# Kernel tuning notes

Hardware: AMD Instinct MI355X
Metric: run time of the kernel (lower is better)

## Reference

```python
import jax, jax.numpy as jnp
import numpy as np

N, C, T, V, H, O = 64, 256, 64, 25, 3, 256
D = max(C // 8, 8)  # rel_channels = 32
BN_EPS = 1e-5


def setup_inputs() -> dict:
    key = jax.random.key(0)
    ks = jax.random.split(key, 12)
    x = jax.random.normal(ks[0], (N, C, T, V), jnp.float32)
    # binary skeleton-style prior adjacency per head + derived 2-hop
    rng = np.random.RandomState(0)
    A = (rng.rand(H, V, V) < 0.15).astype(np.float32)
    A2 = np.zeros_like(A)
    for h in range(H):
        A2[h] = np.clip(np.minimum(A[h] @ A[h], 1.0) - A[h], 0.0, 1.0)
    s = 1.0 / np.sqrt(C)
    return {
        "x": x,
        "A_prior": jnp.asarray(A),
        "A_2hop": jnp.asarray(A2),
        "beta": jnp.float32(0.3),
        "lam": jnp.float32(0.5),
        "W_phi": jax.random.normal(ks[1], (H * D, C), jnp.float32) * s,
        "b_phi": jnp.zeros((H * D,), jnp.float32),
        "W_psi": jax.random.normal(ks[2], (H * D, C), jnp.float32) * s,
        "b_psi": jnp.zeros((H * D,), jnp.float32),
        "W_d": jax.random.normal(ks[3], (H, O, C), jnp.float32) * s,
        "b_d": jnp.zeros((H, O), jnp.float32),
        "bn_gamma": jnp.ones((O,), jnp.float32),
        "bn_beta": jnp.zeros((O,), jnp.float32),
        "bn_mean": jax.random.normal(ks[4], (O,), jnp.float32) * 0.1,
        "bn_var": jax.random.uniform(ks[5], (O,), jnp.float32, 0.5, 1.5),
        "W_g": jax.random.normal(ks[6], (O, C), jnp.float32) * s,
        "b_g": jnp.zeros((O,), jnp.float32),
    }


def reference(x, A_prior, A_2hop, beta, lam, W_phi, b_phi, W_psi, b_psi,
              W_d, b_d, bn_gamma, bn_beta, bn_mean, bn_var, W_g, b_g):
    n, c, t, v = x.shape
    h = A_prior.shape[0]
    d = W_phi.shape[0] // h
    scale = d ** -0.5

    def conv1x1_heads(W, b):
        # n c t v -> (n t) h v d
        y = jnp.einsum('nctv,ec->netv', x, W) + b[None, :, None, None]
        return y.reshape(n, h, d, t, v).transpose(0, 3, 1, 4, 2).reshape(n * t, h, v, d)

    phi = conv1x1_heads(W_phi, b_phi)
    psi = conv1x1_heads(W_psi, b_psi)
    A_adapt = jax.nn.softmax(jnp.einsum('bhvd,bhwd->bhvw', phi, psi) * scale, axis=-1)

    lam_c = jnp.clip(lam, 0.0, 1.0)
    A_final = (A_prior + beta * A_2hop)[None] + lam_c * A_adapt  # [(n t), h, v, v]

    feat = x.transpose(0, 2, 3, 1).reshape(n * t, v, c)  # (n t) v c
    z = jnp.einsum('bhvw,bwc->bhvc', A_final, feat)       # per-head aggregation
    out = jnp.einsum('bhvc,hoc->bvo', z, W_d) + jnp.sum(b_d, axis=0)  # sum of per-head 1x1 convs
    out = out.reshape(n, t, v, -1).transpose(0, 3, 1, 2)  # n o t v

    # BatchNorm2d (inference form with running stats)
    inv = jax.lax.rsqrt(bn_var + BN_EPS)
    out = (out - bn_mean[None, :, None, None]) * (inv * bn_gamma)[None, :, None, None] + bn_beta[None, :, None, None]

    gate = jax.nn.sigmoid(jnp.einsum('nctv,oc->notv', x, W_g) + b_g[None, :, None, None])
    out = gate * out + x  # down is identity since in_channels == out_channels
    return jax.nn.relu(out)
```

## Files before the change

### kernel.cpp

```cpp
#include <hip/hip_runtime.h>
#include <math.h>

#define N_ 64
#define C_ 256
#define T_ 64
#define V_ 25
#define H_ 3
#define O_ 256
#define D_ 32
#define HD_ 96

using short8 = __attribute__((ext_vector_type(8))) short;
using f32x4  = __attribute__((ext_vector_type(4))) float;

#define WS_WD   0
#define WS_WG   196608
#define WS_WPHI 262144
#define WS_WPSI 286720

__device__ __forceinline__ unsigned short f2bf(float f) {
    unsigned int u = __float_as_uint(f);
    unsigned int r = (u + 0x7fffu + ((u >> 16) & 1u)) >> 16;
    return (unsigned short)r;
}

__global__ __launch_bounds__(256)
void prep_weights(const float* __restrict__ Wd, const float* __restrict__ Wg,
                  const float* __restrict__ Wphi, const float* __restrict__ Wpsi,
                  unsigned short* __restrict__ ws) {
    int gid = blockIdx.x * 256 + threadIdx.x;
    if (gid >= 608 * 64) return;
    int tile = gid >> 6, lane = gid & 63;
    int lcol = lane & 15, lrow = lane >> 4;
    const float* W;
    unsigned short* base;
    int ot, ks;
    if (tile < 384) {
        int h = tile >> 7, r = tile & 127;
        ot = r >> 3; ks = r & 7;
        W = Wd + (size_t)h * O_ * C_;
        base = ws + WS_WD + (size_t)tile * 512;
    } else if (tile < 512) {
        int r = tile - 384;
        ot = r >> 3; ks = r & 7;
        W = Wg;
        base = ws + WS_WG + (size_t)r * 512;
    } else if (tile < 560) {
        int r = tile - 512;
        ot = r >> 3; ks = r & 7;
        W = Wphi;
        base = ws + WS_WPHI + (size_t)r * 512;
    } else {
        int r = tile - 560;
        ot = r >> 3; ks = r & 7;
        W = Wpsi;
        base = ws + WS_WPSI + (size_t)r * 512;
    }
    int row = ot * 16 + lcol;
    int c0  = ks * 32 + lrow * 8;
    const float* s = W + (size_t)row * C_ + c0;
    unsigned int p[4];
    #pragma unroll
    for (int q = 0; q < 4; ++q) {
        unsigned short lo = f2bf(s[2 * q]);
        unsigned short hi = f2bf(s[2 * q + 1]);
        p[q] = (unsigned int)lo | ((unsigned int)hi << 16);
    }
    uint4 pk = make_uint4(p[0], p[1], p[2], p[3]);
    *(uint4*)(base + (size_t)lane * 8) = pk;
}

#define L_PHIT 16384
#define L_PSIT 26384
#define L_AFIN 36384
#define L_M    42528
#define L_TOT  63008

__global__ __launch_bounds__(256)
void hdgc_mfma(const float* __restrict__ x,
               const float* __restrict__ A_prior,
               const float* __restrict__ A_2hop,
               const float* __restrict__ beta_p,
               const float* __restrict__ lam_p,
               const float* __restrict__ b_phi,
               const float* __restrict__ b_psi,
               const unsigned short* __restrict__ ws,
               const float* __restrict__ b_d,
               const float* __restrict__ bn_gamma,
               const float* __restrict__ bn_beta,
               const float* __restrict__ bn_mean,
               const float* __restrict__ bn_var,
               const float* __restrict__ b_g,
               float* __restrict__ out) {
    __shared__ __align__(16) char lds[L_TOT];
    char*  xbT  = lds;
    float* phiT = (float*)(lds + L_PHIT);
    float* psiT = (float*)(lds + L_PSIT);
    char*  Afin = lds + L_AFIN;
    char*  Mlds = lds + L_M;
    float* Slds = (float*)(lds + L_M);

    const int tid  = threadIdx.x;
    const int lane = tid & 63, wid = tid >> 6;
    const int lcol = lane & 15, lrow = lane >> 4;
    const int b = blockIdx.x, n = b / T_, t = b - n * T_;
    const size_t xbase = (size_t)n * (C_ * T_ * V_) + (size_t)t * V_;

    for (int i = tid; i < 7 * 256; i += 256) {
        int v = 25 + (i >> 8), c = i & 255;
        *(unsigned short*)(xbT + (((v << 9) + (c << 1)) ^ ((v & 7) << 4))) = 0;
    }
    for (int i = tid; i < 3 * 32 * 32; i += 256)
        ((unsigned short*)Afin)[i] = 0;
    for (int i = tid; i < C_ * V_; i += 256) {
        int c = i / V_, v = i - c * V_;
        unsigned short bv = f2bf(x[xbase + (size_t)c * (T_ * V_) + v]);
        *(unsigned short*)(xbT + (((v << 9) + (c << 1)) ^ ((v & 7) << 4))) = bv;
    }
    __syncthreads();

    {
        const unsigned short* wsrc = ws + ((wid >> 1) ? WS_WPSI : WS_WPHI);
        const float* bias = (wid >> 1) ? b_psi : b_phi;
        float* dstT = (wid >> 1) ? psiT : phiT;
        int otbase = (wid & 1) * 3;
        f32x4 acc[3][2];
        #pragma unroll
        for (int oi = 0; oi < 3; ++oi)
            #pragma unroll
            for (int wt = 0; wt < 2; ++wt) acc[oi][wt] = (f32x4){0.f, 0.f, 0.f, 0.f};
        for (int ks = 0; ks < 8; ++ks) {
            const int cb = (ks * 32 + lrow * 8) << 1;
            short8 b0 = *(const short8*)(xbT + (((lcol << 9) + cb) ^ ((lcol & 7) << 4)));
            const int v1 = 16 + lcol;
            short8 b1 = *(const short8*)(xbT + (((v1 << 9) + cb) ^ ((v1 & 7) << 4)));
            #pragma unroll
            for (int oi = 0; oi < 3; ++oi) {
                int ot = otbase + oi;
                short8 a = *(const short8*)(wsrc + (((ot << 3) + ks) << 9) + lane * 8);
                acc[oi][0] = __builtin_amdgcn_mfma_f32_16x16x32_bf16(a, b0, acc[oi][0], 0, 0, 0);
                acc[oi][1] = __builtin_amdgcn_mfma_f32_16x16x32_bf16(a, b1, acc[oi][1], 0, 0, 0);
            }
        }
        #pragma unroll
        for (int oi = 0; oi < 3; ++oi) {
            int ot = otbase + oi;
            #pragma unroll
            for (int r = 0; r < 4; ++r) {
                int e = ot * 16 + lrow * 4 + r;
                float bv = bias[e];
                if (lcol < 25)      dstT[lcol * 100 + e]       = acc[oi][0][r] + bv;
                if (16 + lcol < 25) dstT[(16 + lcol) * 100 + e] = acc[oi][1][r] + bv;
            }
        }
    }
    __syncthreads();

    for (int it = tid; it < H_ * V_ * V_; it += 256) {
        int h = it / (V_ * V_), rem = it - h * V_ * V_;
        int v = rem / V_, w = rem - v * V_;
        const f32x4* pv = (const f32x4*)(phiT + v * 100 + h * 32);
        const f32x4* pw = (const f32x4*)(psiT + w * 100 + h * 32);
        float s = 0.f;
        #pragma unroll
        for (int q = 0; q < 8; ++q) {
            f32x4 a = pv[q], c = pw[q];
            s += a[0] * c[0] + a[1] * c[1] + a[2] * c[2] + a[3] * c[3];
        }
        Slds[(h * 25 + v) * 28 + w] = s * 0.17677669529663687f;
    }
    __syncthreads();

    if (tid < H_ * V_) {
        int h = tid / 25, v = tid - h * 25;
        float lam  = fminf(fmaxf(lam_p[0], 0.f), 1.f);
        float beta = beta_p[0];
        const float* row = Slds + tid * 28;
        float mx = -1e30f;
        #pragma unroll
        for (int w = 0; w < 25; ++w) mx = fmaxf(mx, row[w]);
        float e[25], sum = 0.f;
        #pragma unroll
        for (int w = 0; w < 25; ++w) { e[w] = __expf(row[w] - mx); sum += e[w]; }
        float sc = lam / sum;
        const float* Ap = A_prior + tid * 25;
        const float* A2 = A_2hop + tid * 25;
        #pragma unroll
        for (int w = 0; w < 25; ++w) {
            float af = Ap[w] + beta * A2[w] + sc * e[w];
            *(unsigned short*)(Afin + (((((h * 32 + v) << 6) + (w << 1))) ^ ((v & 7) << 4))) = f2bf(af);
        }
    }
    __syncthreads();

    f32x4 oacc[4][2], gacc[4][2];
    #pragma unroll
    for (int oi = 0; oi < 4; ++oi)
        #pragma unroll
        for (int vt = 0; vt < 2; ++vt) {
            oacc[oi][vt] = (f32x4){0.f, 0.f, 0.f, 0.f};
            gacc[oi][vt] = (f32x4){0.f, 0.f, 0.f, 0.f};
        }

    for (int h = 0; h < H_; ++h) {
        f32x4 macc[4][2];
        #pragma unroll
        for (int oi = 0; oi < 4; ++oi)
            #pragma unroll
            for (int wt = 0; wt < 2; ++wt) macc[oi][wt] = (f32x4){0.f, 0.f, 0.f, 0.f};
        for (int ks = 0; ks < 8; ++ks) {
            const int cb = (ks * 32 + lrow * 8) << 1;
            short8 b0 = *(const short8*)(xbT + (((lcol << 9) + cb) ^ ((lcol & 7) << 4)));
            const int v1 = 16 + lcol;
            short8 b1 = *(const short8*)(xbT + (((v1 << 9) + cb) ^ ((v1 & 7) << 4)));
            #pragma unroll
            for (int oi = 0; oi < 4; ++oi) {
                int ot = wid * 4 + oi;
                short8 a = *(const short8*)(ws + WS_WD + ((((h * 16 + ot) << 3) + ks) << 9) + lane * 8);
                macc[oi][0] = __builtin_amdgcn_mfma_f32_16x16x32_bf16(a, b0, macc[oi][0], 0, 0, 0);
                macc[oi][1] = __builtin_amdgcn_mfma_f32_16x16x32_bf16(a, b1, macc[oi][1], 0, 0, 0);
            }
        }
        #pragma unroll
        for (int oi = 0; oi < 4; ++oi) {
            int ot = wid * 4 + oi;
            #pragma unroll
            for (int r = 0; r < 4; ++r) {
                int o = ot * 16 + lrow * 4 + r;
                *(unsigned short*)(Mlds + o * 80 + (lcol << 1))        = f2bf(macc[oi][0][r]);
                *(unsigned short*)(Mlds + o * 80 + ((16 + lcol) << 1)) = f2bf(macc[oi][1][r]);
            }
        }
        __syncthreads();
        {
            short8 af[4];
            #pragma unroll
            for (int oi = 0; oi < 4; ++oi) {
                int ot = wid * 4 + oi;
                af[oi] = *(const short8*)(Mlds + (ot * 16 + lcol) * 80 + (lrow << 4));
            }
            #pragma unroll
            for (int vt = 0; vt < 2; ++vt) {
                int v = vt * 16 + lcol;
                short8 bf = *(const short8*)(Afin + ((((h * 32 + v) << 6) + (lrow << 4)) ^ ((v & 7) << 4)));
                #pragma unroll
                for (int oi = 0; oi < 4; ++oi)
                    oacc[oi][vt] = __builtin_amdgcn_mfma_f32_16x16x32_bf16(af[oi], bf, oacc[oi][vt], 0, 0, 0);
            }
        }
        __syncthreads();
    }

    for (int ks = 0; ks < 8; ++ks) {
        const int cb = (ks * 32 + lrow * 8) << 1;
        short8 b0 = *(const short8*)(xbT + (((lcol << 9) + cb) ^ ((lcol & 7) << 4)));
        const int v1 = 16 + lcol;
        short8 b1 = *(const short8*)(xbT + (((v1 << 9) + cb) ^ ((v1 & 7) << 4)));
        #pragma unroll
        for (int oi = 0; oi < 4; ++oi) {
            int ot = wid * 4 + oi;
            short8 a = *(const short8*)(ws + WS_WG + (((ot << 3) + ks) << 9) + lane * 8);
            gacc[oi][0] = __builtin_amdgcn_mfma_f32_16x16x32_bf16(a, b0, gacc[oi][0], 0, 0, 0);
            gacc[oi][1] = __builtin_amdgcn_mfma_f32_16x16x32_bf16(a, b1, gacc[oi][1], 0, 0, 0);
        }
    }

    #pragma unroll
    for (int oi = 0; oi < 4; ++oi) {
        int ot = wid * 4 + oi;
        #pragma unroll
        for (int r = 0; r < 4; ++r) {
            int o = ot * 16 + lrow * 4 + r;
            float bdsum = b_d[o] + b_d[O_ + o] + b_d[2 * O_ + o];
            float inv  = rsqrtf(bn_var[o] + 1e-5f) * bn_gamma[o];
            float mean = bn_mean[o], bnb = bn_beta[o], bg = b_g[o];
            float* op = out + xbase + (size_t)o * (T_ * V_);
            #pragma unroll
            for (int vt = 0; vt < 2; ++vt) {
                int v = vt * 16 + lcol;
                if (v < V_) {
                    float pre = (oacc[oi][vt][r] + bdsum - mean) * inv + bnb;
                    float gl  = gacc[oi][vt][r] + bg;
                    float g   = 1.f / (1.f + __expf(-gl));
                    unsigned short xb =
                        *(unsigned short*)(xbT + (((v << 9) + (o << 1)) ^ ((v & 7) << 4)));
                    float res = __uint_as_float(((unsigned int)xb) << 16);
                    float rr = g * pre + res;
                    op[v] = fmaxf(rr, 0.f);
                }
            }
        }
    }
}

extern "C" void kernel_launch(void* const* d_in, const int* in_sizes, int n_in,
                              void* d_out, int out_size, void* d_ws, size_t ws_size,
                              hipStream_t stream) {
    const float* x        = (const float*)d_in[0];
    const float* A_prior  = (const float*)d_in[1];
    const float* A_2hop   = (const float*)d_in[2];
    const float* beta_p   = (const float*)d_in[3];
    const float* lam_p    = (const float*)d_in[4];
    const float* W_phi    = (const float*)d_in[5];
    const float* b_phi    = (const float*)d_in[6];
    const float* W_psi    = (const float*)d_in[7];
    const float* b_psi    = (const float*)d_in[8];
    const float* W_d      = (const float*)d_in[9];
    const float* b_d      = (const float*)d_in[10];
    const float* bn_gamma = (const float*)d_in[11];
    const float* bn_beta  = (const float*)d_in[12];
    const float* bn_mean  = (const float*)d_in[13];
    const float* bn_var   = (const float*)d_in[14];
    const float* W_g      = (const float*)d_in[15];
    const float* b_g      = (const float*)d_in[16];
    unsigned short* ws = (unsigned short*)d_ws;
    float* out = (float*)d_out;

    hipLaunchKernelGGL(prep_weights, dim3(152), dim3(256), 0, stream,
                       W_d, W_g, W_phi, W_psi, ws);
    hipLaunchKernelGGL(hdgc_mfma, dim3(N_ * T_), dim3(256), 0, stream,
                       x, A_prior, A_2hop, beta_p, lam_p,
                       b_phi, b_psi, ws,
                       b_d, bn_gamma, bn_beta, bn_mean, bn_var, b_g, out);
}
```

Before: 464.6 us.

## Compute phi·psi scores with bf16 MFMA and shrink LDS footprint

Stores phi/psi projections as bf16 in a shared scratch region and computes the per-head 25x25 attention scores with four 16x16x32 bf16 MFMAs per head, replacing the scalar fp32 dot-product loop. The LDS layout is compacted by overlapping the phi/psi/score scratch with the later M buffer, which reduces per-block shared memory and may allow more resident blocks. The x staging loop now packs two channels per 32-bit store. Rounding phi/psi to bf16 adds precision loss in the softmax logits.

After: 515.0 us. 1.11x slower.

```diff
diff --git a/kernel.cpp b/kernel.cpp
--- a/kernel.cpp
+++ b/kernel.cpp
@@ -70,11 +70,13 @@
     *(uint4*)(base + (size_t)lane * 8) = pk;
 }
 
-#define L_PHIT 16384
-#define L_PSIT 26384
-#define L_AFIN 36384
-#define L_M    42528
-#define L_TOT  63008
+#define L_AFIN 16384
+#define L_SCR  22528
+#define L_PHIB L_SCR
+#define L_PSIB (L_SCR + 6656)
+#define L_S    (L_SCR + 13312)
+#define L_M    L_SCR
+#define L_TOT  44240
 
 __global__ __launch_bounds__(256)
 void hdgc_mfma(const float* __restrict__ x,
@@ -93,12 +95,12 @@
                const float* __restrict__ b_g,
                float* __restrict__ out) {
     __shared__ __align__(16) char lds[L_TOT];
-    char*  xbT  = lds;
-    float* phiT = (float*)(lds + L_PHIT);
-    float* psiT = (float*)(lds + L_PSIT);
-    char*  Afin = lds + L_AFIN;
-    char*  Mlds = lds + L_M;
-    float* Slds = (float*)(lds + L_M);
+    char*           xbT  = lds;
+    char*           Afin = lds + L_AFIN;
+    unsigned short* phiB = (unsigned short*)(lds + L_PHIB);
+    unsigned short* psiB = (unsigned short*)(lds + L_PSIB);
+    float*          Slds = (float*)(lds + L_S);
+    char*           Mlds = lds + L_M;
 
     const int tid  = threadIdx.x;
     const int lane = tid & 63, wid = tid >> 6;
@@ -112,17 +114,20 @@
     }
     for (int i = tid; i < 3 * 32 * 32; i += 256)
         ((unsigned short*)Afin)[i] = 0;
-    for (int i = tid; i < C_ * V_; i += 256) {
-        int c = i / V_, v = i - c * V_;
-        unsigned short bv = f2bf(x[xbase + (size_t)c * (T_ * V_) + v]);
-        *(unsigned short*)(xbT + (((v << 9) + (c << 1)) ^ ((v & 7) << 4))) = bv;
+    for (int i = tid; i < 128 * V_; i += 256) {
+        int p = i / V_, v = i - p * V_;
+        int c = p * 2;
+        const float* xs = x + xbase + (size_t)c * (T_ * V_) + v;
+        unsigned int lo = f2bf(xs[0]);
+        unsigned int hi = f2bf(xs[T_ * V_]);
+        *(unsigned int*)(xbT + (((v << 9) + (c << 1)) ^ ((v & 7) << 4))) = lo | (hi << 16);
     }
     __syncthreads();
 
     {
         const unsigned short* wsrc = ws + ((wid >> 1) ? WS_WPSI : WS_WPHI);
         const float* bias = (wid >> 1) ? b_psi : b_phi;
-        float* dstT = (wid >> 1) ? psiT : phiT;
+        unsigned short* dstB = (wid >> 1) ? psiB : phiB;
         int otbase = (wid & 1) * 3;
         f32x4 acc[3][2];
         #pragma unroll
@@ -149,25 +154,40 @@
             for (int r = 0; r < 4; ++r) {
                 int e = ot * 16 + lrow * 4 + r;
                 float bv = bias[e];
-                if (lcol < 25)      dstT[lcol * 100 + e]       = acc[oi][0][r] + bv;
-                if (16 + lcol < 25) dstT[(16 + lcol) * 100 + e] = acc[oi][1][r] + bv;
+                if (lcol < 25) dstB[lcol * 104 + e]        = f2bf(acc[oi][0][r] + bv);
+                if (lcol < 9)  dstB[(16 + lcol) * 104 + e] = f2bf(acc[oi][1][r] + bv);
             }
         }
     }
     __syncthreads();
 
-    for (int it = tid; it < H_ * V_ * V_; it += 256) {
-        int h = it / (V_ * V_), rem = it - h * V_ * V_;
-        int v = rem / V_, w = rem - v * V_;
-        const f32x4* pv = (const f32x4*)(phiT + v * 100 + h * 32);
-        const f32x4* pw = (const f32x4*)(psiT + w * 100 + h * 32);
-        float s = 0.f;
-        #pragma unroll
-        for (int q = 0; q < 8; ++q) {
-            f32x4 a = pv[q], c = pw[q];
-            s += a[0] * c[0] + a[1] * c[1] + a[2] * c[2] + a[3] * c[3];
-        }
-        Slds[(h * 25 + v) * 28 + w] = s * 0.17677669529663687f;
+    if (wid < H_) {
+        const int h = wid;
+        const int eo = h * 32 + lrow * 8;
+        short8 a0 = *(const short8*)(phiB + lcol * 104 + eo);
+        short8 a1 = *(const short8*)(phiB + (16 + lcol) * 104 + eo);
+        short8 q0 = *(const short8*)(psiB + lcol * 104 + eo);
+        short8 q1 = *(const short8*)(psiB + (16 + lcol) * 104 + eo);
+        f32x4 s00 = (f32x4){0.f, 0.f, 0.f, 0.f}, s01 = s00, s10 = s00, s11 = s00;
+        s00 = __builtin_amdgcn_mfma_f32_16x16x32_bf16(a0, q0, s00, 0, 0, 0);
+        s01 = __builtin_amdgcn_mfma_f32_16x16x32_bf16(a0, q1, s01, 0, 0, 0);
+        s10 = __builtin_amdgcn_mfma_f32_16x16x32_bf16(a1, q0, s10, 0, 0, 0);
+        s11 = __builtin_amdgcn_mfma_f32_16x16x32_bf16(a1, q1, s11, 0, 0, 0);
+        const float scf = 0.17677669529663687f;
+        #pragma unroll
+        for (int r = 0; r < 4; ++r) {
+            int v0 = lrow * 4 + r, v1 = 16 + v0;
+            if (v0 < 25) {
+                float* row = Slds + (h * 25 + v0) * 28;
+                row[lcol] = s00[r] * scf;
+                if (16 + lcol < 25) row[16 + lcol] = s01[r] * scf;
+            }
+            if (v1 < 25) {
+                float* row = Slds + (h * 25 + v1) * 28;
+                row[lcol] = s10[r] * scf;
+                if (16 + lcol < 25) row[16 + lcol] = s11[r] * scf;
+            }
+        }
     }
     __syncthreads();
 
```
